# Kernel optimization log

Hardware: AMD Instinct MI355X
Metric: run time of the kernel (lower is better)

## Reference

```python
import jax, jax.numpy as jnp
import numpy as np

P_FLIP, P_COLOR, P_ERASE = 0.5, 0.7, 0.3
B, C, H, W = 256, 3, 224, 224


def setup_inputs() -> dict:
    key = jax.random.key(0)
    ks = jax.random.split(key, 8)
    return {
        "x": jax.random.uniform(ks[0], (B, C, H, W), dtype=jnp.float32),
        "flip_u": jax.random.uniform(ks[1], (B,), dtype=jnp.float32),
        "bright_u": jax.random.uniform(ks[2], (B,), dtype=jnp.float32),
        "bright_v": jax.random.uniform(ks[3], (B,), dtype=jnp.float32),
        "contrast_u": jax.random.uniform(ks[4], (B,), dtype=jnp.float32),
        "contrast_v": jax.random.uniform(ks[5], (B,), dtype=jnp.float32),
        "erase_u": jax.random.uniform(ks[6], (B,), dtype=jnp.float32),
        "erase_box_u": jax.random.uniform(ks[7], (B, 4), dtype=jnp.float32),
    }


def _augment(x, flip_u, bright_u, bright_v, contrast_u, contrast_v, erase_u, erase_box_u):
    b, c, h, w = x.shape
    # horizontal flip (last dim) on masked samples
    fm = (flip_u < P_FLIP)[:, None, None, None]
    x = jnp.where(fm, x[..., ::-1], x)
    # brightness: scale by 0.8 + 0.4*u on masked samples
    bm = (bright_u < P_COLOR)[:, None, None, None]
    bval = (0.8 + 0.4 * bright_v)[:, None, None, None]
    x = jnp.where(bm, x * bval, x)
    # contrast: (x - mean)*c + mean with per-sample mean over C,H,W
    cm = (contrast_u < P_COLOR)[:, None, None, None]
    cval = (0.8 + 0.4 * contrast_v)[:, None, None, None]
    mean = jnp.mean(x, axis=(1, 2, 3), keepdims=True)
    x = jnp.where(cm, (x - mean) * cval + mean, x)
    # random erase: zero a per-sample box; int() truncation matched by floor
    em = erase_u < P_ERASE
    eh = jnp.floor(h * (0.02 + 0.18 * erase_box_u[:, 0])).astype(jnp.int32)
    ew = jnp.floor(w * (0.02 + 0.18 * erase_box_u[:, 1])).astype(jnp.int32)
    ph = jnp.floor((h - eh).astype(jnp.float32) * erase_box_u[:, 2]).astype(jnp.int32)
    pw = jnp.floor((w - ew).astype(jnp.float32) * erase_box_u[:, 3]).astype(jnp.int32)
    rows = jnp.arange(h, dtype=jnp.int32)[None, :]  # [1,H]
    cols = jnp.arange(w, dtype=jnp.int32)[None, :]  # [1,W]
    rmask = (rows >= ph[:, None]) & (rows < (ph + eh)[:, None])  # [B,H]
    wmask = (cols >= pw[:, None]) & (cols < (pw + ew)[:, None])  # [B,W]
    box = rmask[:, None, :, None] & wmask[:, None, None, :] & em[:, None, None, None]
    x = jnp.where(box, jnp.zeros((), x.dtype), x)
    return jnp.clip(x, 0.0, 1.0)


def reference(x, flip_u, bright_u, bright_v, contrast_u, contrast_v, erase_u, erase_box_u):
    return _augment(x, flip_u, bright_u, bright_v, contrast_u, contrast_v, erase_u, erase_box_u)
```

## Files before the change

kernel.cpp:

```cpp
#include <hip/hip_runtime.h>
#include <math.h>

#define NB    256
#define NC    3
#define NH    224
#define NW    224
#define SAMPLE_ELEMS (NC * NH * NW)
#define SAMPLE_V4    (SAMPLE_ELEMS / 4)
#define BLOCKS_PER_SAMPLE 8
#define CHUNK_V4 (SAMPLE_V4 / BLOCKS_PER_SAMPLE)
#define W4 (NW / 4)

struct SampleParams {
    float s;
    float t;
    int   flip;
    int   em;
    int   ph, ph_end, pw, pw_end;
};

__global__ __launch_bounds__(256) void sum_kernel(const float4* __restrict__ x,
                                                  float* __restrict__ partials) {
    const int b = blockIdx.x / BLOCKS_PER_SAMPLE;
    const int j = blockIdx.x % BLOCKS_PER_SAMPLE;
    const float4* base = x + (size_t)b * SAMPLE_V4 + (size_t)j * CHUNK_V4;

    float s = 0.0f;
    for (int k = threadIdx.x; k < CHUNK_V4; k += 256) {
        float4 v = base[k];
        s += (v.x + v.y) + (v.z + v.w);
    }
    #pragma unroll
    for (int off = 32; off > 0; off >>= 1) s += __shfl_down(s, off, 64);

    __shared__ float red[4];
    const int lane = threadIdx.x & 63;
    const int wid  = threadIdx.x >> 6;
    if (lane == 0) red[wid] = s;
    __syncthreads();
    if (threadIdx.x == 0)
        partials[blockIdx.x] = (red[0] + red[1]) + (red[2] + red[3]);
}

__global__ __launch_bounds__(256) void params_kernel(
        const float* __restrict__ partials,
        const float* __restrict__ flip_u,
        const float* __restrict__ bright_u,
        const float* __restrict__ bright_v,
        const float* __restrict__ contrast_u,
        const float* __restrict__ contrast_v,
        const float* __restrict__ erase_u,
        const float* __restrict__ erase_box,
        SampleParams* __restrict__ prm) {
    const int b = threadIdx.x;

    float sum = 0.0f;
    #pragma unroll
    for (int j = 0; j < BLOCKS_PER_SAMPLE; ++j) sum += partials[b * BLOCKS_PER_SAMPLE + j];

    const float bsc  = (bright_u[b] < 0.7f) ? (0.8f + 0.4f * bright_v[b]) : 1.0f;
    const float mean = (sum / (float)SAMPLE_ELEMS) * bsc;

    float csc, t;
    if (contrast_u[b] < 0.7f) {
        csc = 0.8f + 0.4f * contrast_v[b];
        t   = mean * (1.0f - csc);
    } else {
        csc = 1.0f;
        t   = 0.0f;
    }

    SampleParams p;
    p.s    = bsc * csc;
    p.t    = t;
    p.flip = (flip_u[b] < 0.5f) ? 1 : 0;
    p.em   = (erase_u[b] < 0.3f) ? 1 : 0;

    const float u0 = erase_box[b * 4 + 0];
    const float u1 = erase_box[b * 4 + 1];
    const float u2 = erase_box[b * 4 + 2];
    const float u3 = erase_box[b * 4 + 3];
    const int eh = (int)floorf((float)NH * (0.02f + 0.18f * u0));
    const int ew = (int)floorf((float)NW * (0.02f + 0.18f * u1));
    const int ph = (int)floorf((float)(NH - eh) * u2);
    const int pw = (int)floorf((float)(NW - ew) * u3);
    p.ph = ph; p.ph_end = ph + eh;
    p.pw = pw; p.pw_end = pw + ew;

    prm[b] = p;
}

__global__ __launch_bounds__(256) void apply_kernel(const float* __restrict__ x,
                                                    const SampleParams* __restrict__ prm,
                                                    float* __restrict__ out) {
    const int i   = blockIdx.x * 256 + threadIdx.x;
    const int w4  = i % W4;
    const int row = i / W4;
    const int h   = row % NH;
    const int b   = row / (NC * NH);

    const SampleParams p = prm[b];

    const int    w0      = w4 * 4;
    const float* src_row = x + (size_t)row * NW;

    float4 v;
    if (p.flip) {
        const float4 r = *(const float4*)(src_row + (NW - 4 - w0));
        v = make_float4(r.w, r.z, r.y, r.x);
    } else {
        v = *(const float4*)(src_row + w0);
    }

    const float s = p.s, t = p.t;
    float o0 = v.x * s + t;
    float o1 = v.y * s + t;
    float o2 = v.z * s + t;
    float o3 = v.w * s + t;

    if (p.em && h >= p.ph && h < p.ph_end) {
        if (w0     >= p.pw && w0     < p.pw_end) o0 = 0.0f;
        if (w0 + 1 >= p.pw && w0 + 1 < p.pw_end) o1 = 0.0f;
        if (w0 + 2 >= p.pw && w0 + 2 < p.pw_end) o2 = 0.0f;
        if (w0 + 3 >= p.pw && w0 + 3 < p.pw_end) o3 = 0.0f;
    }

    o0 = fminf(fmaxf(o0, 0.0f), 1.0f);
    o1 = fminf(fmaxf(o1, 0.0f), 1.0f);
    o2 = fminf(fmaxf(o2, 0.0f), 1.0f);
    o3 = fminf(fmaxf(o3, 0.0f), 1.0f);

    ((float4*)out)[i] = make_float4(o0, o1, o2, o3);
}

extern "C" void kernel_launch(void* const* d_in, const int* in_sizes, int n_in,
                              void* d_out, int out_size, void* d_ws, size_t ws_size,
                              hipStream_t stream) {
    const float* x          = (const float*)d_in[0];
    const float* flip_u     = (const float*)d_in[1];
    const float* bright_u   = (const float*)d_in[2];
    const float* bright_v   = (const float*)d_in[3];
    const float* contrast_u = (const float*)d_in[4];
    const float* contrast_v = (const float*)d_in[5];
    const float* erase_u    = (const float*)d_in[6];
    const float* erase_box  = (const float*)d_in[7];
    float* out = (float*)d_out;

    float*        partials = (float*)d_ws;
    SampleParams* prm      = (SampleParams*)((char*)d_ws + NB * BLOCKS_PER_SAMPLE * sizeof(float));

    sum_kernel<<<NB * BLOCKS_PER_SAMPLE, 256, 0, stream>>>((const float4*)x, partials);
    params_kernel<<<1, 256, 0, stream>>>(partials, flip_u, bright_u, bright_v,
                                         contrast_u, contrast_v, erase_u, erase_box, prm);

    const int total_v4 = NB * SAMPLE_V4;
    apply_kernel<<<total_v4 / 256, 256, 0, stream>>>(x, prm, out);
}
```

Measured before the change: 310.4 us.

## Fuse sum, parameter, and apply kernels into one per-sample block kernel

Replaces the three-kernel pipeline (partial sums, per-sample params, elementwise apply) with a single kernel where one 1024-thread block handles one sample. The block reduces the sample mean in shared memory, computes augmentation parameters locally, then re-reads the sample to apply them. This removes two launches and the workspace round trip, and it relies on the sample being cached for the second read. In exchange, the grid drops to 256 blocks, roughly one per CU, which limits latency hiding.

```diff
diff --git a/kernel.cpp b/kernel.cpp
--- a/kernel.cpp
+++ b/kernel.cpp
@@ -7,43 +7,11 @@
 #define NW    224
 #define SAMPLE_ELEMS (NC * NH * NW)
 #define SAMPLE_V4    (SAMPLE_ELEMS / 4)
-#define BLOCKS_PER_SAMPLE 8
-#define CHUNK_V4 (SAMPLE_V4 / BLOCKS_PER_SAMPLE)
 #define W4 (NW / 4)
+#define THREADS 1024
 
-struct SampleParams {
-    float s;
-    float t;
-    int   flip;
-    int   em;
-    int   ph, ph_end, pw, pw_end;
-};
-
-__global__ __launch_bounds__(256) void sum_kernel(const float4* __restrict__ x,
-                                                  float* __restrict__ partials) {
-    const int b = blockIdx.x / BLOCKS_PER_SAMPLE;
-    const int j = blockIdx.x % BLOCKS_PER_SAMPLE;
-    const float4* base = x + (size_t)b * SAMPLE_V4 + (size_t)j * CHUNK_V4;
-
-    float s = 0.0f;
-    for (int k = threadIdx.x; k < CHUNK_V4; k += 256) {
-        float4 v = base[k];
-        s += (v.x + v.y) + (v.z + v.w);
-    }
-    #pragma unroll
-    for (int off = 32; off > 0; off >>= 1) s += __shfl_down(s, off, 64);
-
-    __shared__ float red[4];
-    const int lane = threadIdx.x & 63;
-    const int wid  = threadIdx.x >> 6;
-    if (lane == 0) red[wid] = s;
-    __syncthreads();
-    if (threadIdx.x == 0)
-        partials[blockIdx.x] = (red[0] + red[1]) + (red[2] + red[3]);
-}
-
-__global__ __launch_bounds__(256) void params_kernel(
-        const float* __restrict__ partials,
+__global__ __launch_bounds__(THREADS) void fused_aug_kernel(
+        const float4* __restrict__ x,
         const float* __restrict__ flip_u,
         const float* __restrict__ bright_u,
         const float* __restrict__ bright_v,
@@ -51,30 +19,52 @@
         const float* __restrict__ contrast_v,
         const float* __restrict__ erase_u,
         const float* __restrict__ erase_box,
-        SampleParams* __restrict__ prm) {
-    const int b = threadIdx.x;
+        float4* __restrict__ out) {
+    const int b = blockIdx.x;
+    const float4* __restrict__ xs = x + (size_t)b * SAMPLE_V4;
+    float4* __restrict__       os = out + (size_t)b * SAMPLE_V4;
 
-    float sum = 0.0f;
+    float s0 = 0.0f, s1 = 0.0f;
+    int k = threadIdx.x;
+    for (; k + THREADS < SAMPLE_V4; k += 2 * THREADS) {
+        float4 a = xs[k];
+        float4 c = xs[k + THREADS];
+        s0 += (a.x + a.y) + (a.z + a.w);
+        s1 += (c.x + c.y) + (c.z + c.w);
+    }
+    if (k < SAMPLE_V4) {
+        float4 a = xs[k];
+        s0 += (a.x + a.y) + (a.z + a.w);
+    }
+    float s = s0 + s1;
+
     #pragma unroll
-    for (int j = 0; j < BLOCKS_PER_SAMPLE; ++j) sum += partials[b * BLOCKS_PER_SAMPLE + j];
+    for (int off = 32; off > 0; off >>= 1) s += __shfl_down(s, off, 64);
+
+    __shared__ float red[16];
+    __shared__ float mean_sh;
+    const int lane = threadIdx.x & 63;
+    const int wid  = threadIdx.x >> 6;
+    if (lane == 0) red[wid] = s;
+    __syncthreads();
+    if (threadIdx.x == 0) {
+        float t = 0.0f;
+        #pragma unroll
+        for (int i = 0; i < 16; ++i) t += red[i];
+        mean_sh = t / (float)SAMPLE_ELEMS;
+    }
+    __syncthreads();
 
     const float bsc  = (bright_u[b] < 0.7f) ? (0.8f + 0.4f * bright_v[b]) : 1.0f;
-    const float mean = (sum / (float)SAMPLE_ELEMS) * bsc;
-
-    float csc, t;
+    const float mean = mean_sh * bsc;
+    float csc = 1.0f, t = 0.0f;
     if (contrast_u[b] < 0.7f) {
         csc = 0.8f + 0.4f * contrast_v[b];
         t   = mean * (1.0f - csc);
-    } else {
-        csc = 1.0f;
-        t   = 0.0f;
     }
-
-    SampleParams p;
-    p.s    = bsc * csc;
-    p.t    = t;
-    p.flip = (flip_u[b] < 0.5f) ? 1 : 0;
-    p.em   = (erase_u[b] < 0.3f) ? 1 : 0;
+    const float scale = bsc * csc;
+    const int   flip  = (flip_u[b] < 0.5f) ? 1 : 0;
+    const int   em    = (erase_u[b] < 0.3f) ? 1 : 0;
 
     const float u0 = erase_box[b * 4 + 0];
     const float u1 = erase_box[b * 4 + 1];
@@ -84,53 +74,42 @@
     const int ew = (int)floorf((float)NW * (0.02f + 0.18f * u1));
     const int ph = (int)floorf((float)(NH - eh) * u2);
     const int pw = (int)floorf((float)(NW - ew) * u3);
-    p.ph = ph; p.ph_end = ph + eh;
-    p.pw = pw; p.pw_end = pw + ew;
+    const int ph_end = ph + eh;
+    const int pw_end = pw + ew;
 
-    prm[b] = p;
-}
+    for (int i = threadIdx.x; i < SAMPLE_V4; i += THREADS) {
+        const int w4  = i % W4;
+        const int row = i / W4;
+        const int h   = row % NH;
+        const int w0  = w4 * 4;
 
-__global__ __launch_bounds__(256) void apply_kernel(const float* __restrict__ x,
-                                                    const SampleParams* __restrict__ prm,
-                                                    float* __restrict__ out) {
-    const int i   = blockIdx.x * 256 + threadIdx.x;
-    const int w4  = i % W4;
-    const int row = i / W4;
-    const int h   = row % NH;
-    const int b   = row / (NC * NH);
+        float4 v;
+        if (flip) {
+            const float4 r = xs[row * W4 + (W4 - 1 - w4)];
+            v = make_float4(r.w, r.z, r.y, r.x);
+        } else {
+            v = xs[i];
+        }
 
-    const SampleParams p = prm[b];
+        float o0 = v.x * scale + t;
+        float o1 = v.y * scale + t;
+        float o2 = v.z * scale + t;
+        float o3 = v.w * scale + t;
 
-    const int    w0      = w4 * 4;
-    const float* src_row = x + (size_t)row * NW;
+        if (em && h >= ph && h < ph_end) {
+            if (w0     >= pw && w0     < pw_end) o0 = 0.0f;
+            if (w0 + 1 >= pw && w0 + 1 < pw_end) o1 = 0.0f;
+            if (w0 + 2 >= pw && w0 + 2 < pw_end) o2 = 0.0f;
+            if (w0 + 3 >= pw && w0 + 3 < pw_end) o3 = 0.0f;
+        }
 
-    float4 v;
-    if (p.flip) {
-        const float4 r = *(const float4*)(src_row + (NW - 4 - w0));
-        v = make_float4(r.w, r.z, r.y, r.x);
-    } else {
-        v = *(const float4*)(src_row + w0);
+        o0 = fminf(fmaxf(o0, 0.0f), 1.0f);
+        o1 = fminf(fmaxf(o1, 0.0f), 1.0f);
+        o2 = fminf(fmaxf(o2, 0.0f), 1.0f);
+        o3 = fminf(fmaxf(o3, 0.0f), 1.0f);
+
+        os[i] = make_float4(o0, o1, o2, o3);
     }
-
-    const float s = p.s, t = p.t;
-    float o0 = v.x * s + t;
-    float o1 = v.y * s + t;
-    float o2 = v.z * s + t;
-    float o3 = v.w * s + t;
-
-    if (p.em && h >= p.ph && h < p.ph_end) {
-        if (w0     >= p.pw && w0     < p.pw_end) o0 = 0.0f;
-        if (w0 + 1 >= p.pw && w0 + 1 < p.pw_end) o1 = 0.0f;
-        if (w0 + 2 >= p.pw && w0 + 2 < p.pw_end) o2 = 0.0f;
-        if (w0 + 3 >= p.pw && w0 + 3 < p.pw_end) o3 = 0.0f;
-    }
-
-    o0 = fminf(fmaxf(o0, 0.0f), 1.0f);
-    o1 = fminf(fmaxf(o1, 0.0f), 1.0f);
-    o2 = fminf(fmaxf(o2, 0.0f), 1.0f);
-    o3 = fminf(fmaxf(o3, 0.0f), 1.0f);
-
-    ((float4*)out)[i] = make_float4(o0, o1, o2, o3);
 }
 
 extern "C" void kernel_launch(void* const* d_in, const int* in_sizes, int n_in,
@@ -144,15 +123,8 @@
     const float* contrast_v = (const float*)d_in[5];
     const float* erase_u    = (const float*)d_in[6];
     const float* erase_box  = (const float*)d_in[7];
-    float* out = (float*)d_out;
 
-    float*        partials = (float*)d_ws;
-    SampleParams* prm      = (SampleParams*)((char*)d_ws + NB * BLOCKS_PER_SAMPLE * sizeof(float));
-
-    sum_kernel<<<NB * BLOCKS_PER_SAMPLE, 256, 0, stream>>>((const float4*)x, partials);
-    params_kernel<<<1, 256, 0, stream>>>(partials, flip_u, bright_u, bright_v,
-                                         contrast_u, contrast_v, erase_u, erase_box, prm);
-
-    const int total_v4 = NB * SAMPLE_V4;
-    apply_kernel<<<total_v4 / 256, 256, 0, stream>>>(x, prm, out);
+    fused_aug_kernel<<<NB, THREADS, 0, stream>>>(
+        (const float4*)x, flip_u, bright_u, bright_v,
+        contrast_u, contrast_v, erase_u, erase_box, (float4*)d_out);
 }
```

Result: no change. 311.1 us (+0.2%).
